# Optimization experiments

Hardware: AMD Instinct MI355X
Metric: run time of the kernel (lower is better)

The kernel has to match this reference:

```python
import jax, jax.numpy as jnp
import numpy as np

B_SZ = 16
L = 256
D_MODEL = 256
D_STATE = 16
D_CONV = 4
EXPAND = 2
D_INNER = EXPAND * D_MODEL  # 512
DT_RANK = (D_MODEL + 15) // 16  # 16
TARGET_LEN = 16


def setup_inputs() -> dict:
    key = jax.random.key(0)
    ks = jax.random.split(key, 10)
    s = 0.02
    x = jax.random.normal(ks[0], (B_SZ, D_MODEL, L), dtype=jnp.float32)
    W_in = jax.random.normal(ks[1], (2 * D_INNER, D_MODEL), dtype=jnp.float32) * s
    conv_w = jax.random.normal(ks[2], (D_INNER, D_CONV), dtype=jnp.float32) * s
    conv_b = jax.random.normal(ks[3], (D_INNER,), dtype=jnp.float32) * s
    W_x = jax.random.normal(ks[4], (DT_RANK + 2 * D_STATE, D_INNER), dtype=jnp.float32) * s
    W_dt = jax.random.normal(ks[5], (D_INNER, DT_RANK), dtype=jnp.float32) * s
    b_dt = jax.random.normal(ks[6], (D_INNER,), dtype=jnp.float32) * s
    # canonical Mamba A init: A_log = log(1..d_state) per channel
    A_log = jnp.log(jnp.tile(jnp.arange(1, D_STATE + 1, dtype=jnp.float32), (D_INNER, 1)))
    Dp = jnp.ones((D_INNER,), dtype=jnp.float32)
    W_out = jax.random.normal(ks[7], (D_MODEL, D_INNER), dtype=jnp.float32) * s
    return {"x": x, "W_in": W_in, "conv_w": conv_w, "conv_b": conv_b,
            "W_x": W_x, "W_dt": W_dt, "b_dt": b_dt, "A_log": A_log,
            "Dp": Dp, "W_out": W_out}


def _selective_scan(u, delta, A, Bm, Cm, Dp):
    # u, delta: [B,L,d_in]; Bm, Cm: [B,L,N]; A: [d_in,N]; Dp: [d_in]
    dA = jnp.exp(delta[..., None] * A)                                  # [B,L,d_in,N]
    dBu = delta[..., None] * Bm[:, :, None, :] * u[..., None]           # [B,L,d_in,N]

    def step(h, t):
        dA_t, dBu_t, C_t = t                                            # [B,d_in,N],[B,d_in,N],[B,N]
        h = dA_t * h + dBu_t
        y = jnp.einsum('bdn,bn->bd', h, C_t)
        return h, y

    h0 = jnp.zeros((u.shape[0], u.shape[2], A.shape[1]), u.dtype)
    _, ys = jax.lax.scan(step, h0,
                         (dA.transpose(1, 0, 2, 3), dBu.transpose(1, 0, 2, 3),
                          Cm.transpose(1, 0, 2)))
    return ys.transpose(1, 0, 2) + u * Dp                               # [B,L,d_in]


def _mamba(xt, W_in, conv_w, conv_b, W_x, W_dt, b_dt, A_log, Dp, W_out):
    # xt: [B,L,D_MODEL]
    xz = xt @ W_in.T                                                    # [B,L,2*d_in]
    xi, z = jnp.split(xz, 2, axis=-1)
    # causal depthwise conv1d over L
    xc = xi.transpose(0, 2, 1)                                          # [B,d_in,L]
    xc = jax.lax.conv_general_dilated(
        xc, conv_w[:, None, :], (1,), [(D_CONV - 1, 0)],
        dimension_numbers=('NCH', 'OIH', 'NCH'), feature_group_count=D_INNER)
    xi = jax.nn.silu((xc + conv_b[None, :, None]).transpose(0, 2, 1))   # [B,L,d_in]
    x_dbl = xi @ W_x.T                                                  # [B,L,dt_rank+2N]
    dt, Bm, Cm = jnp.split(x_dbl, [DT_RANK, DT_RANK + D_STATE], axis=-1)
    delta = jax.nn.softplus(dt @ W_dt.T + b_dt)                         # [B,L,d_in]
    A = -jnp.exp(A_log)                                                 # [d_in,N]
    y = _selective_scan(xi, delta, A, Bm, Cm, Dp)
    y = y * jax.nn.silu(z)
    return y @ W_out.T                                                  # [B,L,D_MODEL]


def reference(x, W_in, conv_w, conv_b, W_x, W_dt, b_dt, A_log, Dp, W_out):
    inp = x.transpose(0, 2, 1)                                          # [B,L,D]
    outs = []
    for _ in range(TARGET_LEN):
        o = _mamba(inp, W_in, conv_w, conv_b, W_x, W_dt, b_dt, A_log, Dp, W_out)[:, -1:, :]
        outs.append(o)
        inp = jnp.concatenate([inp[:, 1:, :], o], axis=1)
    return jnp.concatenate(outs, axis=1).transpose(0, 2, 1)             # [B,D,target_len]
```

## Files before the change

### kernel.cpp

```cpp
#include <hip/hip_runtime.h>
#include <cmath>

#define DEV __device__ __forceinline__

constexpr int B_SZ = 16;
constexpr int LSEQ = 256;
constexpr int DM   = 256;
constexpr int DI   = 512;
constexpr int NST  = 16;
constexpr int RK   = 16;
constexpr int TLEN = 16;

DEV float silu_f(float x)     { return x / (1.f + __expf(-x)); }
DEV float softplus_f(float x) { return log1pf(__expf(x)); }

__global__ __launch_bounds__(256) void k_inproj(const float* __restrict__ x,
                                                const float* __restrict__ W_in,
                                                float* __restrict__ xi_pre) {
    __shared__ float As[32][68];
    __shared__ float Ws[32][68];
    const int by = blockIdx.y, bx = blockIdx.x;
    const int row0 = by * 64;
    const int b = row0 >> 8, l0 = row0 & 255;
    const int j0 = bx * 64;
    const int tid = threadIdx.x;
    const int ty = tid >> 4, tx = tid & 15;
    const float* xb = x + (size_t)b * DM * LSEQ;
    float acc[4][4] = {};
    for (int kc = 0; kc < DM; kc += 32) {
        for (int it = 0; it < 8; ++it) {
            int idx = it * 256 + tid;
            int kk = idx >> 6, li = idx & 63;
            As[kk][li] = xb[(kc + kk) * LSEQ + l0 + li];
        }
        for (int it = 0; it < 8; ++it) {
            int idx = it * 256 + tid;
            int jj = idx >> 5, kk = idx & 31;
            Ws[kk][jj] = W_in[(j0 + jj) * DM + kc + kk];
        }
        __syncthreads();
        for (int kk = 0; kk < 32; ++kk) {
            float4 a4 = *(const float4*)&As[kk][ty * 4];
            float4 w4 = *(const float4*)&Ws[kk][tx * 4];
            float av[4] = {a4.x, a4.y, a4.z, a4.w};
            float wv[4] = {w4.x, w4.y, w4.z, w4.w};
            for (int i = 0; i < 4; ++i)
                for (int j = 0; j < 4; ++j) acc[i][j] = fmaf(av[i], wv[j], acc[i][j]);
        }
        __syncthreads();
    }
    for (int i = 0; i < 4; ++i) {
        float4 v = make_float4(acc[i][0], acc[i][1], acc[i][2], acc[i][3]);
        *(float4*)&xi_pre[(size_t)(row0 + ty * 4 + i) * DI + j0 + tx * 4] = v;
    }
}

__global__ void k_z255(const float* __restrict__ x, const float* __restrict__ W_in,
                       float* __restrict__ z255) {
    const int b = blockIdx.x, tid = threadIdx.x;
    const float* xb = x + (size_t)b * DM * LSEQ;
    for (int jj = tid; jj < DI; jj += 256) {
        const float* wr = W_in + (size_t)(DI + jj) * DM;
        float s = 0.f;
        for (int k = 0; k < DM; ++k) s = fmaf(xb[k * LSEQ + 255], wr[k], s);
        z255[b * DI + jj] = s;
    }
}

__global__ __launch_bounds__(512) void k_conv(const float* __restrict__ xi_pre,
                                              const float* __restrict__ conv_w,
                                              const float* __restrict__ conv_b,
                                              float* __restrict__ xi) {
    const int bl = blockIdx.x;
    const int l = bl & 255;
    const int d = threadIdx.x;
    float s = conv_b[d];
    for (int k = 0; k < 4; ++k) {
        int ll = l - 3 + k;
        if (ll >= 0) s = fmaf(conv_w[d * 4 + k], xi_pre[(size_t)(bl - 3 + k) * DI + d], s);
    }
    xi[(size_t)bl * DI + d] = silu_f(s);
}

__global__ void k_dtbc(const float* __restrict__ xi, const float* __restrict__ W_x,
                       float* __restrict__ dtBC) {
    const int row = blockIdx.x;
    const int j = threadIdx.x;
    if (j < 48) {
        const float* wr = W_x + (size_t)j * DI;
        const float* xr = xi + (size_t)row * DI;
        float s = 0.f;
        for (int k = 0; k < DI; ++k) s = fmaf(xr[k], wr[k], s);
        dtBC[row * 48 + j] = s;
    }
}

__global__ __launch_bounds__(512) void k_scan_chunk(const float* __restrict__ xi,
                                                    const float* __restrict__ dtBC,
                                                    const float* __restrict__ W_dt,
                                                    const float* __restrict__ b_dt,
                                                    const float* __restrict__ A_log,
                                                    float* __restrict__ Qb,
                                                    float* __restrict__ Sb) {
    const int blk = blockIdx.x;
    const int b = blk >> 3, c = blk & 7;
    const int d = threadIdx.x;
    float Ar[16], Wd[16];
    for (int n = 0; n < 16; ++n) Ar[n] = -__expf(A_log[d * 16 + n]);
    for (int r = 0; r < 16; ++r) Wd[r] = W_dt[d * 16 + r];
    const float bd = b_dt[d];
    float q[16] = {};
    float Ssum = 0.f;
    for (int l = c * 32; l < c * 32 + 32; ++l) {
        const int rl = b * 256 + l;
        const float* dv = dtBC + (size_t)rl * 48;
        float s = bd;
        for (int r = 0; r < 16; ++r) s = fmaf(dv[r], Wd[r], s);
        const float del = softplus_f(s);
        const float u = xi[(size_t)rl * DI + d];
        const float du = del * u;
        Ssum += del;
        for (int n = 0; n < 16; ++n) {
            float dA = __expf(del * Ar[n]);
            q[n] = fmaf(dA, q[n], du * dv[16 + n]);
        }
    }
    float* qo = Qb + ((size_t)blk * DI + d) * 16;
    for (int n = 0; n < 16; ++n) qo[n] = q[n];
    Sb[blk * DI + d] = Ssum;
}

__global__ __launch_bounds__(512) void k_compose(const float* __restrict__ Qb,
                                                 const float* __restrict__ Sb,
                                                 const float* __restrict__ dtBC,
                                                 const float* __restrict__ xi,
                                                 const float* __restrict__ z255,
                                                 const float* __restrict__ A_log,
                                                 const float* __restrict__ Dp,
                                                 float* __restrict__ h_state,
                                                 float* __restrict__ gbuf) {
    const int b = blockIdx.x;
    const int d = threadIdx.x;
    float Ar[16];
    for (int n = 0; n < 16; ++n) Ar[n] = -__expf(A_log[d * 16 + n]);
    float h[16] = {};
    for (int c = 0; c < 8; ++c) {
        const int blk = b * 8 + c;
        const float S = Sb[blk * DI + d];
        const float* qv = Qb + ((size_t)blk * DI + d) * 16;
        for (int n = 0; n < 16; ++n) {
            float P = __expf(S * Ar[n]);
            h[n] = fmaf(P, h[n], qv[n]);
        }
    }
    const float* Cv = dtBC + (size_t)(b * 256 + 255) * 48 + 32;
    float y = 0.f;
    for (int n = 0; n < 16; ++n) y = fmaf(h[n], Cv[n], y);
    const float u = xi[(size_t)(b * 256 + 255) * DI + d];
    y = fmaf(u, Dp[d], y);
    gbuf[b * DI + d] = y * silu_f(z255[b * DI + d]);
    float* ho = h_state + ((size_t)(b * DI + d)) * 16;
    for (int n = 0; n < 16; ++n) ho[n] = h[n];
}

DEV void group_barrier(unsigned* flag, unsigned target) {
    __syncthreads();
    if (threadIdx.x == 0) {
        __hip_atomic_fetch_add(flag, 1u, __ATOMIC_ACQ_REL, __HIP_MEMORY_SCOPE_AGENT);
        while (__hip_atomic_load(flag, __ATOMIC_ACQUIRE, __HIP_MEMORY_SCOPE_AGENT) < target) {
            __builtin_amdgcn_s_sleep(2);
        }
    }
    __syncthreads();
}

__global__ __launch_bounds__(256) void k_gen(
    const float* __restrict__ W_in, const float* __restrict__ conv_w,
    const float* __restrict__ conv_b, const float* __restrict__ W_x,
    const float* __restrict__ W_dt, const float* __restrict__ b_dt,
    const float* __restrict__ A_log, const float* __restrict__ Dp,
    const float* __restrict__ W_out, const float* __restrict__ xi_pre,
    const float* __restrict__ h_state, const float* __restrict__ gbuf0,
    float* __restrict__ o_part, float* __restrict__ dt_part,
    unsigned* __restrict__ bar, float* __restrict__ out) {
    const int bid = blockIdx.x;
    const int b = bid & 15;
    const int p = bid >> 4;
    const int d0 = p * 64;
    const int tid = threadIdx.x;

    __shared__ float gs[64];
    __shared__ float os[256];
    __shared__ float hist[3][64];
    __shared__ float xin[64];
    __shared__ float zs[64];
    __shared__ float dtbc[48];
    __shared__ float red[256];

    const int dl = tid >> 2, nq = tid & 3;
    const int dg = d0 + dl;

    float h[4], Ar[4];
    {
        const float* hs = h_state + ((size_t)(b * DI + dg)) * 16 + nq * 4;
        for (int j = 0; j < 4; ++j) h[j] = hs[j];
        for (int j = 0; j < 4; ++j) Ar[j] = -__expf(A_log[dg * 16 + nq * 4 + j]);
    }
    if (tid < 64) {
        gs[tid] = gbuf0[b * DI + d0 + tid];
        for (int k = 0; k < 3; ++k)
            hist[k][tid] = xi_pre[(size_t)(b * 256 + 253 + k) * DI + d0 + tid];
    }
    __syncthreads();

    unsigned* mybar = bar + b;
    unsigned nb = 0;

    for (int t = 0; t < TLEN; ++t) {
        {
            const float* wr = W_out + (size_t)tid * DI + d0;
            float s = 0.f;
            for (int dd = 0; dd < 64; ++dd) s = fmaf(wr[dd], gs[dd], s);
            __hip_atomic_store(&o_part[(b * 8 + p) * 256 + tid], s,
                               __ATOMIC_RELAXED, __HIP_MEMORY_SCOPE_AGENT);
        }
        ++nb; group_barrier(mybar, 8u * nb);

        {
            float s = 0.f;
            for (int pp = 0; pp < 8; ++pp)
                s += __hip_atomic_load(&o_part[(b * 8 + pp) * 256 + tid],
                                       __ATOMIC_RELAXED, __HIP_MEMORY_SCOPE_AGENT);
            os[tid] = s;
            if (p == 0) out[(b * 256 + tid) * TLEN + t] = s;
        }
        __syncthreads();
        if (t == TLEN - 1) return;

        {
            const int jj = tid >> 1, half = tid & 1;
            const int jglob = (jj < 64) ? (d0 + jj) : (DI + d0 + (jj - 64));
            const float* wr = W_in + (size_t)jglob * DM + half * 128;
            const float* ov = os + half * 128;
            float s = 0.f;
            for (int k = 0; k < 128; ++k) s = fmaf(wr[k], ov[k], s);
            red[tid] = s;
        }
        __syncthreads();
        if (tid < 128) {
            const int jj = tid;
            float v = red[2 * jj] + red[2 * jj + 1];
            if (jj < 64) {
                const int d = d0 + jj;
                float xc = conv_b[d];
                xc = fmaf(conv_w[d * 4 + 0], hist[t % 3][jj], xc);
                xc = fmaf(conv_w[d * 4 + 1], hist[(t + 1) % 3][jj], xc);
                xc = fmaf(conv_w[d * 4 + 2], hist[(t + 2) % 3][jj], xc);
                xc = fmaf(conv_w[d * 4 + 3], v, xc);
                hist[t % 3][jj] = v;
                xin[jj] = silu_f(xc);
            } else {
                zs[jj - 64] = v;
            }
        }
        __syncthreads();
        if (tid < 192) {
            const int r = tid >> 2, q4 = tid & 3;
            const float* wr = W_x + (size_t)r * DI + d0 + q4 * 16;
            const float* xv = xin + q4 * 16;
            float s = 0.f;
            for (int k = 0; k < 16; ++k) s = fmaf(wr[k], xv[k], s);
            red[tid] = s;
        }
        __syncthreads();
        if (tid < 48) {
            float v = red[4 * tid] + red[4 * tid + 1] + red[4 * tid + 2] + red[4 * tid + 3];
            __hip_atomic_store(&dt_part[(b * 8 + p) * 48 + tid], v,
                               __ATOMIC_RELAXED, __HIP_MEMORY_SCOPE_AGENT);
        }
        ++nb; group_barrier(mybar, 8u * nb);

        if (tid < 48) {
            float s = 0.f;
            for (int pp = 0; pp < 8; ++pp)
                s += __hip_atomic_load(&dt_part[(b * 8 + pp) * 48 + tid],
                                       __ATOMIC_RELAXED, __HIP_MEMORY_SCOPE_AGENT);
            dtbc[tid] = s;
        }
        __syncthreads();
        {
            float dt_l = b_dt[dg];
            for (int r = 0; r < 16; ++r) dt_l = fmaf(dtbc[r], W_dt[dg * 16 + r], dt_l);
            const float del = softplus_f(dt_l);
            const float u = xin[dl];
            const float du = del * u;
            float y = 0.f;
            for (int j = 0; j < 4; ++j) {
                const int n = nq * 4 + j;
                float dA = __expf(del * Ar[j]);
                h[j] = fmaf(dA, h[j], du * dtbc[16 + n]);
                y = fmaf(h[j], dtbc[32 + n], y);
            }
            y += __shfl_xor(y, 1);
            y += __shfl_xor(y, 2);
            if (nq == 0) {
                float yt = fmaf(u, Dp[dg], y);
                gs[dl] = yt * silu_f(zs[dl]);
            }
        }
        __syncthreads();
    }
}

extern "C" void kernel_launch(void* const* d_in, const int* in_sizes, int n_in,
                              void* d_out, int out_size, void* d_ws, size_t ws_size,
                              hipStream_t stream) {
    const float* x      = (const float*)d_in[0];
    const float* W_in   = (const float*)d_in[1];
    const float* conv_w = (const float*)d_in[2];
    const float* conv_b = (const float*)d_in[3];
    const float* W_x    = (const float*)d_in[4];
    const float* W_dt   = (const float*)d_in[5];
    const float* b_dt   = (const float*)d_in[6];
    const float* A_log  = (const float*)d_in[7];
    const float* Dp     = (const float*)d_in[8];
    const float* W_out  = (const float*)d_in[9];
    float* out = (float*)d_out;

    float* base = (float*)d_ws;
    size_t off = 0;
    auto alloc = [&](size_t n) { float* pp = base + off; off += (n + 15) & ~(size_t)15; return pp; };
    unsigned* bar   = (unsigned*)alloc(64);
    float* o_part   = alloc(16 * 8 * 256);
    float* dt_part  = alloc(16 * 8 * 48);
    float* gbuf     = alloc(16 * 512);
    float* h_state  = alloc((size_t)16 * 512 * 16);
    float* z255     = alloc(16 * 512);
    float* dtBC     = alloc((size_t)4096 * 48);
    float* Sb       = alloc((size_t)128 * 512);
    float* Qb       = alloc((size_t)128 * 512 * 16);
    float* xi_pre   = alloc((size_t)4096 * 512);
    float* xi       = alloc((size_t)4096 * 512);

    hipMemsetAsync(bar, 0, 256, stream);
    hipLaunchKernelGGL(k_inproj, dim3(8, 64), dim3(256), 0, stream, x, W_in, xi_pre);
    hipLaunchKernelGGL(k_z255, dim3(16), dim3(256), 0, stream, x, W_in, z255);
    hipLaunchKernelGGL(k_conv, dim3(4096), dim3(512), 0, stream, xi_pre, conv_w, conv_b, xi);
    hipLaunchKernelGGL(k_dtbc, dim3(4096), dim3(64), 0, stream, xi, W_x, dtBC);
    hipLaunchKernelGGL(k_scan_chunk, dim3(128), dim3(512), 0, stream,
                       xi, dtBC, W_dt, b_dt, A_log, Qb, Sb);
    hipLaunchKernelGGL(k_compose, dim3(16), dim3(512), 0, stream,
                       Qb, Sb, dtBC, xi, z255, A_log, Dp, h_state, gbuf);
    hipLaunchKernelGGL(k_gen, dim3(128), dim3(256), 0, stream,
                       W_in, conv_w, conv_b, W_x, W_dt, b_dt, A_log, Dp, W_out,
                       xi_pre, h_state, gbuf, o_part, dt_part, bar, out);
}
```

Measured before the change: 409.8 us.

## Tile dtbc GEMM, parallelize z255, split gen across 256 blocks with smem-cached weights

Rewrites k_dtbc as a shared-memory tiled GEMM over 32-row tiles instead of one 48-thread dot product per row. k_z255 becomes a wave-reduction kernel over 64 blocks. k_gen moves to 256 blocks of 32 channels each and caches its W_in, W_out, W_x and W_dt slices in shared memory. This removes repeated global weight reads across the 16 decode steps. In exchange each cross-block barrier now waits on 16 blocks instead of 8, the partial sums to combine double, and shared-memory use per block becomes large.

```diff
diff --git a/kernel.cpp b/kernel.cpp
--- a/kernel.cpp
+++ b/kernel.cpp
@@ -7,8 +7,6 @@
 constexpr int LSEQ = 256;
 constexpr int DM   = 256;
 constexpr int DI   = 512;
-constexpr int NST  = 16;
-constexpr int RK   = 16;
 constexpr int TLEN = 16;
 
 DEV float silu_f(float x)     { return x / (1.f + __expf(-x)); }
@@ -55,15 +53,22 @@
     }
 }
 
-__global__ void k_z255(const float* __restrict__ x, const float* __restrict__ W_in,
-                       float* __restrict__ z255) {
-    const int b = blockIdx.x, tid = threadIdx.x;
-    const float* xb = x + (size_t)b * DM * LSEQ;
-    for (int jj = tid; jj < DI; jj += 256) {
-        const float* wr = W_in + (size_t)(DI + jj) * DM;
-        float s = 0.f;
-        for (int k = 0; k < DM; ++k) s = fmaf(xb[k * LSEQ + 255], wr[k], s);
-        z255[b * DI + jj] = s;
+__global__ __launch_bounds__(256) void k_z255(const float* __restrict__ x,
+                                              const float* __restrict__ W_in,
+                                              float* __restrict__ z255) {
+    __shared__ __align__(16) float xcol[256];
+    const int b = blockIdx.x >> 2, jq = blockIdx.x & 3;
+    const int tid = threadIdx.x;
+    xcol[tid] = x[(size_t)b * DM * LSEQ + tid * LSEQ + 255];
+    __syncthreads();
+    const int w = tid >> 6, lane = tid & 63;
+    float4 xv = *(const float4*)&xcol[lane * 4];
+    for (int rr = 0; rr < 32; ++rr) {
+        const int j = jq * 128 + w * 32 + rr;
+        float4 wv = *(const float4*)&W_in[(size_t)(DI + j) * DM + lane * 4];
+        float s = wv.x * xv.x + wv.y * xv.y + wv.z * xv.z + wv.w * xv.w;
+        for (int off = 32; off > 0; off >>= 1) s += __shfl_down(s, off);
+        if (lane == 0) z255[b * DI + j] = s;
     }
 }
 
@@ -82,17 +87,36 @@
     xi[(size_t)bl * DI + d] = silu_f(s);
 }
 
-__global__ void k_dtbc(const float* __restrict__ xi, const float* __restrict__ W_x,
-                       float* __restrict__ dtBC) {
-    const int row = blockIdx.x;
-    const int j = threadIdx.x;
-    if (j < 48) {
-        const float* wr = W_x + (size_t)j * DI;
-        const float* xr = xi + (size_t)row * DI;
-        float s = 0.f;
-        for (int k = 0; k < DI; ++k) s = fmaf(xr[k], wr[k], s);
-        dtBC[row * 48 + j] = s;
-    }
+__global__ __launch_bounds__(256) void k_dtbc(const float* __restrict__ xi,
+                                              const float* __restrict__ W_x,
+                                              float* __restrict__ dtBC) {
+    __shared__ float As[32][65];
+    __shared__ float Ws[48][65];
+    const int row0 = blockIdx.x * 32;
+    const int tid = threadIdx.x;
+    const int r = tid >> 3, cg = tid & 7;
+    float acc[6] = {};
+    for (int kc = 0; kc < DI; kc += 64) {
+        for (int it = 0; it < 8; ++it) {
+            int idx = it * 256 + tid;
+            int rr = idx >> 6, k = idx & 63;
+            As[rr][k] = xi[(size_t)(row0 + rr) * DI + kc + k];
+        }
+        for (int it = 0; it < 12; ++it) {
+            int idx = it * 256 + tid;
+            int c = idx >> 6, k = idx & 63;
+            Ws[c][k] = W_x[(size_t)c * DI + kc + k];
+        }
+        __syncthreads();
+        for (int kk = 0; kk < 64; ++kk) {
+            float a = As[r][kk];
+            for (int ci = 0; ci < 6; ++ci)
+                acc[ci] = fmaf(a, Ws[cg * 6 + ci][kk], acc[ci]);
+        }
+        __syncthreads();
+    }
+    for (int ci = 0; ci < 6; ++ci)
+        dtBC[(size_t)(row0 + r) * 48 + cg * 6 + ci] = acc[ci];
 }
 
 __global__ __launch_bounds__(512) void k_scan_chunk(const float* __restrict__ xi,
@@ -174,7 +198,7 @@
     __syncthreads();
 }
 
-__global__ __launch_bounds__(256) void k_gen(
+__global__ __launch_bounds__(256, 1) void k_gen(
     const float* __restrict__ W_in, const float* __restrict__ conv_w,
     const float* __restrict__ conv_b, const float* __restrict__ W_x,
     const float* __restrict__ W_dt, const float* __restrict__ b_dt,
@@ -186,50 +210,79 @@
     const int bid = blockIdx.x;
     const int b = bid & 15;
     const int p = bid >> 4;
-    const int d0 = p * 64;
+    const int d0 = p * 32;
     const int tid = threadIdx.x;
 
-    __shared__ float gs[64];
+    __shared__ float win_s[64][257];
+    __shared__ float wout_s[256][33];
+    __shared__ float wx_s[48][33];
+    __shared__ float wdt_s[32][17];
     __shared__ float os[256];
-    __shared__ float hist[3][64];
-    __shared__ float xin[64];
-    __shared__ float zs[64];
-    __shared__ float dtbc[48];
     __shared__ float red[256];
-
-    const int dl = tid >> 2, nq = tid & 3;
-    const int dg = d0 + dl;
-
-    float h[4], Ar[4];
+    __shared__ float gs[32], xin[32], zs[32], dtbc[48];
+    __shared__ float hist[3][32];
+
+    for (int it = 0; it < 64; ++it) {
+        int idx = it * 256 + tid;
+        int r = idx >> 8, k = idx & 255;
+        int jglob = (r < 32) ? (d0 + r) : (DI + d0 + (r - 32));
+        win_s[r][k] = W_in[(size_t)jglob * DM + k];
+    }
+    for (int it = 0; it < 32; ++it) {
+        int idx = it * 256 + tid;
+        int m = idx >> 5, dd = idx & 31;
+        wout_s[m][dd] = W_out[(size_t)m * DI + d0 + dd];
+    }
+    for (int it = 0; it < 6; ++it) {
+        int idx = it * 256 + tid;
+        int r = idx >> 5, dd = idx & 31;
+        wx_s[r][dd] = W_x[(size_t)r * DI + d0 + dd];
+    }
+    for (int it = 0; it < 2; ++it) {
+        int idx = it * 256 + tid;
+        int j = idx >> 4, n = idx & 15;
+        wdt_s[j][n] = W_dt[(size_t)(d0 + j) * 16 + n];
+    }
+
+    const int dsc = tid >> 3, np = tid & 7, nn = np * 2;
+    const int dg = d0 + dsc;
+    float h[2], Ar[2];
     {
-        const float* hs = h_state + ((size_t)(b * DI + dg)) * 16 + nq * 4;
-        for (int j = 0; j < 4; ++j) h[j] = hs[j];
-        for (int j = 0; j < 4; ++j) Ar[j] = -__expf(A_log[dg * 16 + nq * 4 + j]);
-    }
-    if (tid < 64) {
-        gs[tid] = gbuf0[b * DI + d0 + tid];
+        const float* hs = h_state + ((size_t)(b * DI + dg)) * 16 + nn;
+        h[0] = hs[0]; h[1] = hs[1];
+        Ar[0] = -__expf(A_log[dg * 16 + nn]);
+        Ar[1] = -__expf(A_log[dg * 16 + nn + 1]);
+    }
+    const float bd = b_dt[dg];
+    const float Dpv = Dp[dg];
+    float cw0 = 0, cw1 = 0, cw2 = 0, cw3 = 0, cb = 0;
+    if (tid < 32) {
+        const int d = d0 + tid;
+        cw0 = conv_w[d * 4 + 0]; cw1 = conv_w[d * 4 + 1];
+        cw2 = conv_w[d * 4 + 2]; cw3 = conv_w[d * 4 + 3];
+        cb = conv_b[d];
+        gs[tid] = gbuf0[b * DI + d];
         for (int k = 0; k < 3; ++k)
-            hist[k][tid] = xi_pre[(size_t)(b * 256 + 253 + k) * DI + d0 + tid];
+            hist[k][tid] = xi_pre[(size_t)(b * 256 + 253 + k) * DI + d];
     }
     __syncthreads();
 
-    unsigned* mybar = bar + b;
+    unsigned* mybar = bar + b * 32;
     unsigned nb = 0;
 
     for (int t = 0; t < TLEN; ++t) {
         {
-            const float* wr = W_out + (size_t)tid * DI + d0;
             float s = 0.f;
-            for (int dd = 0; dd < 64; ++dd) s = fmaf(wr[dd], gs[dd], s);
-            __hip_atomic_store(&o_part[(b * 8 + p) * 256 + tid], s,
+            for (int dd = 0; dd < 32; ++dd) s = fmaf(wout_s[tid][dd], gs[dd], s);
+            __hip_atomic_store(&o_part[(b * 16 + p) * 256 + tid], s,
                                __ATOMIC_RELAXED, __HIP_MEMORY_SCOPE_AGENT);
         }
-        ++nb; group_barrier(mybar, 8u * nb);
+        ++nb; group_barrier(mybar, 16u * nb);
 
         {
             float s = 0.f;
-            for (int pp = 0; pp < 8; ++pp)
-                s += __hip_atomic_load(&o_part[(b * 8 + pp) * 256 + tid],
+            for (int pp = 0; pp < 16; ++pp)
+                s += __hip_atomic_load(&o_part[(b * 16 + pp) * 256 + tid],
                                        __ATOMIC_RELAXED, __HIP_MEMORY_SCOPE_AGENT);
             os[tid] = s;
             if (p == 0) out[(b * 256 + tid) * TLEN + t] = s;
@@ -238,74 +291,69 @@
         if (t == TLEN - 1) return;
 
         {
-            const int jj = tid >> 1, half = tid & 1;
-            const int jglob = (jj < 64) ? (d0 + jj) : (DI + d0 + (jj - 64));
-            const float* wr = W_in + (size_t)jglob * DM + half * 128;
-            const float* ov = os + half * 128;
+            const int j = tid & 63, q = tid >> 6;
             float s = 0.f;
-            for (int k = 0; k < 128; ++k) s = fmaf(wr[k], ov[k], s);
+            for (int kk = 0; kk < 64; ++kk) s = fmaf(win_s[j][q * 64 + kk], os[q * 64 + kk], s);
             red[tid] = s;
         }
         __syncthreads();
-        if (tid < 128) {
-            const int jj = tid;
-            float v = red[2 * jj] + red[2 * jj + 1];
-            if (jj < 64) {
-                const int d = d0 + jj;
-                float xc = conv_b[d];
-                xc = fmaf(conv_w[d * 4 + 0], hist[t % 3][jj], xc);
-                xc = fmaf(conv_w[d * 4 + 1], hist[(t + 1) % 3][jj], xc);
-                xc = fmaf(conv_w[d * 4 + 2], hist[(t + 2) % 3][jj], xc);
-                xc = fmaf(conv_w[d * 4 + 3], v, xc);
-                hist[t % 3][jj] = v;
-                xin[jj] = silu_f(xc);
+        if (tid < 64) {
+            const int j = tid;
+            float v = red[j] + red[64 + j] + red[128 + j] + red[192 + j];
+            if (j < 32) {
+                float xc = cb;
+                xc = fmaf(cw0, hist[t % 3][j], xc);
+                xc = fmaf(cw1, hist[(t + 1) % 3][j], xc);
+                xc = fmaf(cw2, hist[(t + 2) % 3][j], xc);
+                xc = fmaf(cw3, v, xc);
+                hist[t % 3][j] = v;
+                xin[j] = silu_f(xc);
             } else {
-                zs[jj - 64] = v;
+                zs[j - 32] = v;
             }
         }
         __syncthreads();
         if (tid < 192) {
-            const int r = tid >> 2, q4 = tid & 3;
-            const float* wr = W_x + (size_t)r * DI + d0 + q4 * 16;
-            const float* xv = xin + q4 * 16;
+            const int r = tid >> 2, q = tid & 3;
             float s = 0.f;
-            for (int k = 0; k < 16; ++k) s = fmaf(wr[k], xv[k], s);
+            for (int kk = 0; kk < 8; ++kk) s = fmaf(wx_s[r][q * 8 + kk], xin[q * 8 + kk], s);
             red[tid] = s;
         }
         __syncthreads();
         if (tid < 48) {
             float v = red[4 * tid] + red[4 * tid + 1] + red[4 * tid + 2] + red[4 * tid + 3];
-            __hip_atomic_store(&dt_part[(b * 8 + p) * 48 + tid], v,
+            __hip_atomic_store(&dt_part[(b * 16 + p) * 48 + tid], v,
                                __ATOMIC_RELAXED, __HIP_MEMORY_SCOPE_AGENT);
         }
-        ++nb; group_barrier(mybar, 8u * nb);
+        ++nb; group_barrier(mybar, 16u * nb);
 
         if (tid < 48) {
             float s = 0.f;
-            for (int pp = 0; pp < 8; ++pp)
-                s += __hip_atomic_load(&dt_part[(b * 8 + pp) * 48 + tid],
+            for (int pp = 0; pp < 16; ++pp)
+                s += __hip_atomic_load(&dt_part[(b * 16 + pp) * 48 + tid],
                                        __ATOMIC_RELAXED, __HIP_MEMORY_SCOPE_AGENT);
             dtbc[tid] = s;
         }
         __syncthreads();
         {
-            float dt_l = b_dt[dg];
-            for (int r = 0; r < 16; ++r) dt_l = fmaf(dtbc[r], W_dt[dg * 16 + r], dt_l);
+            float dt_l = bd;
+            for (int r = 0; r < 16; ++r) dt_l = fmaf(dtbc[r], wdt_s[dsc][r], dt_l);
             const float del = softplus_f(dt_l);
-            const float u = xin[dl];
+            const float u = xin[dsc];
             const float du = del * u;
             float y = 0.f;
-            for (int j = 0; j < 4; ++j) {
-                const int n = nq * 4 + j;
+            for (int j = 0; j < 2; ++j) {
+                const int n = nn + j;
                 float dA = __expf(del * Ar[j]);
                 h[j] = fmaf(dA, h[j], du * dtbc[16 + n]);
                 y = fmaf(h[j], dtbc[32 + n], y);
             }
             y += __shfl_xor(y, 1);
             y += __shfl_xor(y, 2);
-            if (nq == 0) {
-                float yt = fmaf(u, Dp[dg], y);
-                gs[dl] = yt * silu_f(zs[dl]);
+            y += __shfl_xor(y, 4);
+            if (np == 0) {
+                float yt = fmaf(u, Dpv, y);
+                gs[dsc] = yt * silu_f(zs[dsc]);
             }
         }
         __syncthreads();
@@ -330,9 +378,9 @@
     float* base = (float*)d_ws;
     size_t off = 0;
     auto alloc = [&](size_t n) { float* pp = base + off; off += (n + 15) & ~(size_t)15; return pp; };
-    unsigned* bar   = (unsigned*)alloc(64);
-    float* o_part   = alloc(16 * 8 * 256);
-    float* dt_part  = alloc(16 * 8 * 48);
+    unsigned* bar   = (unsigned*)alloc(16 * 32);
+    float* o_part   = alloc(16 * 16 * 256);
+    float* dt_part  = alloc(16 * 16 * 48);
     float* gbuf     = alloc(16 * 512);
     float* h_state  = alloc((size_t)16 * 512 * 16);
     float* z255     = alloc(16 * 512);
@@ -342,16 +390,16 @@
     float* xi_pre   = alloc((size_t)4096 * 512);
     float* xi       = alloc((size_t)4096 * 512);
 
-    hipMemsetAsync(bar, 0, 256, stream);
+    hipMemsetAsync(bar, 0, 16 * 32 * sizeof(unsigned), stream);
     hipLaunchKernelGGL(k_inproj, dim3(8, 64), dim3(256), 0, stream, x, W_in, xi_pre);
-    hipLaunchKernelGGL(k_z255, dim3(16), dim3(256), 0, stream, x, W_in, z255);
+    hipLaunchKernelGGL(k_z255, dim3(64), dim3(256), 0, stream, x, W_in, z255);
     hipLaunchKernelGGL(k_conv, dim3(4096), dim3(512), 0, stream, xi_pre, conv_w, conv_b, xi);
-    hipLaunchKernelGGL(k_dtbc, dim3(4096), dim3(64), 0, stream, xi, W_x, dtBC);
+    hipLaunchKernelGGL(k_dtbc, dim3(128), dim3(256), 0, stream, xi, W_x, dtBC);
     hipLaunchKernelGGL(k_scan_chunk, dim3(128), dim3(512), 0, stream,
                        xi, dtBC, W_dt, b_dt, A_log, Qb, Sb);
     hipLaunchKernelGGL(k_compose, dim3(16), dim3(512), 0, stream,
                        Qb, Sb, dtBC, xi, z255, A_log, Dp, h_state, gbuf);
-    hipLaunchKernelGGL(k_gen, dim3(128), dim3(256), 0, stream,
+    hipLaunchKernelGGL(k_gen, dim3(256), dim3(256), 0, stream,
                        W_in, conv_w, conv_b, W_x, W_dt, b_dt, A_log, Dp, W_out,
                        xi_pre, h_state, gbuf, o_part, dt_part, bar, out);
 }
```

Result: slower. 424.6 us (+3.6%).
